# Performance work log

Hardware: AMD Instinct MI355X
Metric: run time of the kernel (lower is better)

Reference implementation:

```python
import jax, jax.numpy as jnp
import numpy as np


def setup_inputs() -> dict:
    key = jax.random.key(0)
    ks = jax.random.split(key, 6)
    B, Tq, Tk = 4, 512, 512
    Q, K, C = 1024, 1024, 256
    query = jax.random.normal(ks[0], (B, Tq, Q), dtype=jnp.float32)
    kmat = jax.random.normal(ks[1], (B, Tk, K), dtype=jnp.float32)
    # Linear weights (torch nn.Linear stores [out, in]; we keep [in, out] for einsum)
    Wq = jax.random.normal(ks[2], (Q, C), dtype=jnp.float32) / np.sqrt(Q)
    Wk = jax.random.normal(ks[3], (K, C), dtype=jnp.float32) / np.sqrt(K)
    w_attn = jax.random.normal(ks[4], (C,), dtype=jnp.float32) / np.sqrt(C)
    b_attn = jax.random.normal(ks[5], (), dtype=jnp.float32) * 0.01
    return {"query": query, "key": kmat, "Wq": Wq, "Wk": Wk,
            "w_attn": w_attn, "b_attn": b_attn}


def reference(query, key, Wq, Wk, w_attn, b_attn):
    # Additive (Bahdanau) attention scores.
    # q2ctx: (B, Tq, C); k2ctx: (B, Tk, C)
    q2ctx = jnp.einsum('bqi,ic->bqc', query, Wq)
    k2ctx = jnp.einsum('bki,ic->bkc', key, Wk)
    # broadcast add -> (B, Tq, Tk, C), tanh, project to scalar and squeeze
    ctx = jnp.tanh(q2ctx[:, :, None, :] + k2ctx[:, None, :, :])
    scores = jnp.einsum('bqkc,c->bqk', ctx, w_attn) + b_attn
    return scores  # (B, Tq, Tk)
```

## Files before the change

### kernel.cpp

```cpp
#include <hip/hip_runtime.h>
#include <hip/hip_bf16.h>

#define M_ROWS 2048
#define KDIM   1024
#define CDIM   256
#define TQ     512
#define TK     512

#define GBM 64
#define GBN 32
#define GBK 32

#define SCALE2LOG2E 2.8853900817779268f

typedef __attribute__((ext_vector_type(8))) short short8;
typedef __attribute__((ext_vector_type(8))) unsigned short ushort8;
typedef __attribute__((ext_vector_type(4))) float floatx4;
typedef __attribute__((ext_vector_type(2))) float f32x2;

__device__ __forceinline__ short2 cvt2(float x, float y) {
    __hip_bfloat162 h = __float22bfloat162_rn(make_float2(x, y));
    short2 r;
    __builtin_memcpy(&r, &h, sizeof(r));
    return r;
}
__device__ __forceinline__ unsigned short f2bf1(float x) {
    return (unsigned short)cvt2(x, x).x;
}
__device__ __forceinline__ float bf2f(unsigned short u) {
    return __builtin_bit_cast(float, (unsigned)u << 16);
}
__device__ __forceinline__ f32x2 splat2(float x) { return (f32x2){x, x}; }

__global__ __launch_bounds__(256) void gemm_mfma_kernel(
    const float* __restrict__ Aq, const float* __restrict__ Ak,
    const float* __restrict__ Wq, const float* __restrict__ Wk,
    const float* __restrict__ w_attn,
    unsigned short* __restrict__ Eq, unsigned short* __restrict__ Ek)
{
    __shared__ short Ws[GBN][GBK + 8];

    const int z = blockIdx.z;
    const float* A = z ? Ak : Aq;
    const float* W = z ? Wk : Wq;
    unsigned short* E = z ? Ek : Eq;

    const int t    = threadIdx.x;
    const int lane = t & 63;
    const int wave = t >> 6;
    const int m0   = blockIdx.x * GBM;
    const int n0   = blockIdx.y * GBN;

    const int wr = t >> 3;
    const int wc = (t & 7) * 4;
    const int li = lane & 15;
    const int qd = lane >> 4;

    const int row = m0 + wave * 16 + li;
    const float* Arow = A + (size_t)row * KDIM + qd * 8;

    floatx4 acc0 = {0.f, 0.f, 0.f, 0.f};
    floatx4 acc1 = {0.f, 0.f, 0.f, 0.f};

    float4 pa0[2], pa1[2], pw[2];
    pa0[0] = *(const float4*)&Arow[0];
    pa1[0] = *(const float4*)&Arow[4];
    pw[0]  = *(const float4*)&W[(size_t)wr * CDIM + n0 + wc];
    pa0[1] = *(const float4*)&Arow[GBK];
    pa1[1] = *(const float4*)&Arow[GBK + 4];
    pw[1]  = *(const float4*)&W[(size_t)(GBK + wr) * CDIM + n0 + wc];

    for (int it = 0; it < KDIM / GBK; ++it) {
        const int s = it & 1;
        __syncthreads();
        short2 u0 = cvt2(pw[s].x, pw[s].y), u1 = cvt2(pw[s].z, pw[s].w);
        Ws[wc + 0][wr] = u0.x;
        Ws[wc + 1][wr] = u0.y;
        Ws[wc + 2][wr] = u1.x;
        Ws[wc + 3][wr] = u1.y;
        short2 p0 = cvt2(pa0[s].x, pa0[s].y), p1 = cvt2(pa0[s].z, pa0[s].w);
        short2 p2 = cvt2(pa1[s].x, pa1[s].y), p3 = cvt2(pa1[s].z, pa1[s].w);
        short8 bv = { p0.x, p0.y, p1.x, p1.y, p2.x, p2.y, p3.x, p3.y };
        __syncthreads();
        if (it + 2 < KDIM / GBK) {
            const int k0 = (it + 2) * GBK;
            pa0[s] = *(const float4*)&Arow[k0];
            pa1[s] = *(const float4*)&Arow[k0 + 4];
            pw[s]  = *(const float4*)&W[(size_t)(k0 + wr) * CDIM + n0 + wc];
        }
        short8 af0 = *(const short8*)&Ws[li][qd * 8];
        short8 af1 = *(const short8*)&Ws[16 + li][qd * 8];
        acc0 = __builtin_amdgcn_mfma_f32_16x16x32_bf16(af0, bv, acc0, 0, 0, 0);
        acc1 = __builtin_amdgcn_mfma_f32_16x16x32_bf16(af1, bv, acc1, 0, 0, 0);
    }

    #pragma unroll
    for (int r = 0; r < 4; ++r) {
        const int c0 = n0 + qd * 4 + r;
        const int c1 = c0 + 16;
        float s0 = z ? 1.0f : (-0.5f / w_attn[c0]);
        float s1 = z ? 1.0f : (-0.5f / w_attn[c1]);
        float v0 = __builtin_amdgcn_exp2f(acc0[r] * SCALE2LOG2E) * s0;
        float v1 = __builtin_amdgcn_exp2f(acc1[r] * SCALE2LOG2E) * s1;
        E[(size_t)c0 * M_ROWS + row] = f2bf1(v0);
        E[(size_t)c1 * M_ROWS + row] = f2bf1(v1);
    }
}

__global__ __launch_bounds__(256) void bahdanau_kernel(
    const unsigned short* __restrict__ Eqs, const unsigned short* __restrict__ Ek,
    const float* __restrict__ w_attn, const float* __restrict__ b_attn,
    float* __restrict__ out)
{
    __shared__ float qs[64][36];
    __shared__ float ks[64][36];
    __shared__ __align__(16) float sl[CDIM];
    __shared__ float partial[4];

    const int t  = threadIdx.x;
    const int b  = blockIdx.z;
    const int q0 = blockIdx.x * 32;
    const int k0 = blockIdx.y * 32;
    const int gq = b * TQ + q0;
    const int gk = b * TK + k0;
    const int tq = (t >> 4) * 2;
    const int tk = (t & 15) * 2;

    const int lr = t >> 2;
    const int lc = (t & 3) * 8;

    {
        float wv = w_attn[t];
        sl[t] = -0.5f / wv;
        float sum = wv;
        #pragma unroll
        for (int o = 32; o >= 1; o >>= 1) sum += __shfl_down(sum, o);
        if ((t & 63) == 0) partial[t >> 6] = sum;
    }

    ushort8 qu = *(const ushort8*)&Eqs[(size_t)lr * M_ROWS + gq + lc];
    ushort8 ku = *(const ushort8*)&Ek [(size_t)lr * M_ROWS + gk + lc];

    f32x2 accA = {0.f, 0.f};
    f32x2 accB = {0.f, 0.f};

    for (int ch = 0; ch < 4; ++ch) {
        __syncthreads();
        *(float4*)&qs[lr][lc]     = make_float4(bf2f(qu[0]), bf2f(qu[1]), bf2f(qu[2]), bf2f(qu[3]));
        *(float4*)&qs[lr][lc + 4] = make_float4(bf2f(qu[4]), bf2f(qu[5]), bf2f(qu[6]), bf2f(qu[7]));
        *(float4*)&ks[lr][lc]     = make_float4(bf2f(ku[0]), bf2f(ku[1]), bf2f(ku[2]), bf2f(ku[3]));
        *(float4*)&ks[lr][lc + 4] = make_float4(bf2f(ku[4]), bf2f(ku[5]), bf2f(ku[6]), bf2f(ku[7]));
        __syncthreads();
        if (ch < 3) {
            const int c1 = (ch + 1) * 64;
            qu = *(const ushort8*)&Eqs[(size_t)(c1 + lr) * M_ROWS + gq + lc];
            ku = *(const ushort8*)&Ek [(size_t)(c1 + lr) * M_ROWS + gk + lc];
        }
        const int cb = ch * 64;
        #pragma unroll
        for (int cc = 0; cc < 64; cc += 4) {
            float4 s4 = *(const float4*)&sl[cb + cc];
            f32x2 q1 = *(const f32x2*)&qs[cc + 0][tq];
            f32x2 q2 = *(const f32x2*)&qs[cc + 1][tq];
            f32x2 q3 = *(const f32x2*)&qs[cc + 2][tq];
            f32x2 q4 = *(const f32x2*)&qs[cc + 3][tq];
            f32x2 k1 = *(const f32x2*)&ks[cc + 0][tk];
            f32x2 k2 = *(const f32x2*)&ks[cc + 1][tk];
            f32x2 k3 = *(const f32x2*)&ks[cc + 2][tk];
            f32x2 k4 = *(const f32x2*)&ks[cc + 3][tk];
            {
                f32x2 f1 = __builtin_elementwise_fma(splat2(q1.x), k1, splat2(s4.x));
                f32x2 f2 = __builtin_elementwise_fma(splat2(q2.x), k2, splat2(s4.y));
                f32x2 f3 = __builtin_elementwise_fma(splat2(q3.x), k3, splat2(s4.z));
                f32x2 f4 = __builtin_elementwise_fma(splat2(q4.x), k4, splat2(s4.w));
                f32x2 p12 = f1 * f2, p34 = f3 * f4;
                f32x2 s12 = f1 + f2, s34 = f3 + f4;
                f32x2 num = __builtin_elementwise_fma(s12, p34, s34 * p12);
                f32x2 den = p12 * p34;
                f32x2 r = {__builtin_amdgcn_rcpf(den.x), __builtin_amdgcn_rcpf(den.y)};
                accA = __builtin_elementwise_fma(num, r, accA);
            }
            {
                f32x2 f1 = __builtin_elementwise_fma(splat2(q1.y), k1, splat2(s4.x));
                f32x2 f2 = __builtin_elementwise_fma(splat2(q2.y), k2, splat2(s4.y));
                f32x2 f3 = __builtin_elementwise_fma(splat2(q3.y), k3, splat2(s4.z));
                f32x2 f4 = __builtin_elementwise_fma(splat2(q4.y), k4, splat2(s4.w));
                f32x2 p12 = f1 * f2, p34 = f3 * f4;
                f32x2 s12 = f1 + f2, s34 = f3 + f4;
                f32x2 num = __builtin_elementwise_fma(s12, p34, s34 * p12);
                f32x2 den = p12 * p34;
                f32x2 r = {__builtin_amdgcn_rcpf(den.x), __builtin_amdgcn_rcpf(den.y)};
                accB = __builtin_elementwise_fma(num, r, accB);
            }
        }
    }

    const float bias2 = *b_attn + partial[0] + partial[1] + partial[2] + partial[3];
    float* o = out + ((size_t)b * TQ + q0 + tq) * TK + k0 + tk;
    *(float2*)&o[0]  = make_float2(accA.x + bias2, accA.y + bias2);
    *(float2*)&o[TK] = make_float2(accB.x + bias2, accB.y + bias2);
}

extern "C" void kernel_launch(void* const* d_in, const int* in_sizes, int n_in,
                              void* d_out, int out_size, void* d_ws, size_t ws_size,
                              hipStream_t stream) {
    const float* query  = (const float*)d_in[0];
    const float* key    = (const float*)d_in[1];
    const float* Wq     = (const float*)d_in[2];
    const float* Wk     = (const float*)d_in[3];
    const float* w_attn = (const float*)d_in[4];
    const float* b_attn = (const float*)d_in[5];
    float* out = (float*)d_out;

    unsigned short* Eqs = (unsigned short*)d_ws;
    unsigned short* Ek  = Eqs + (size_t)CDIM * M_ROWS;

    dim3 gemm_grid(M_ROWS / GBM, CDIM / GBN, 2);
    gemm_mfma_kernel<<<gemm_grid, 256, 0, stream>>>(query, key, Wq, Wk, w_attn, Eqs, Ek);

    dim3 main_grid(TQ / 32, TK / 32, 4);
    bahdanau_kernel<<<main_grid, 256, 0, stream>>>(Eqs, Ek, w_attn, b_attn, out);
}
```

Measured before the change: 109.6 us.

## Deepen GEMM prefetch, double-buffer LDS, and split channels across waves in scorer

Result: slower. 112.1 us (+2.3%).

```diff
diff --git a/kernel.cpp b/kernel.cpp
--- a/kernel.cpp
+++ b/kernel.cpp
@@ -10,6 +10,8 @@
 #define GBM 64
 #define GBN 32
 #define GBK 32
+#define NIT (KDIM / GBK)
+#define DEPTH 4
 
 #define SCALE2LOG2E 2.8853900817779268f
 
@@ -38,7 +40,7 @@
     const float* __restrict__ w_attn,
     unsigned short* __restrict__ Eq, unsigned short* __restrict__ Ek)
 {
-    __shared__ short Ws[GBN][GBK + 8];
+    __shared__ short Ws[2][GBN][GBK + 8];
 
     const int z = blockIdx.z;
     const float* A = z ? Ak : Aq;
@@ -62,36 +64,49 @@
     floatx4 acc0 = {0.f, 0.f, 0.f, 0.f};
     floatx4 acc1 = {0.f, 0.f, 0.f, 0.f};
 
-    float4 pa0[2], pa1[2], pw[2];
-    pa0[0] = *(const float4*)&Arow[0];
-    pa1[0] = *(const float4*)&Arow[4];
-    pw[0]  = *(const float4*)&W[(size_t)wr * CDIM + n0 + wc];
-    pa0[1] = *(const float4*)&Arow[GBK];
-    pa1[1] = *(const float4*)&Arow[GBK + 4];
-    pw[1]  = *(const float4*)&W[(size_t)(GBK + wr) * CDIM + n0 + wc];
-
-    for (int it = 0; it < KDIM / GBK; ++it) {
-        const int s = it & 1;
-        __syncthreads();
-        short2 u0 = cvt2(pw[s].x, pw[s].y), u1 = cvt2(pw[s].z, pw[s].w);
-        Ws[wc + 0][wr] = u0.x;
-        Ws[wc + 1][wr] = u0.y;
-        Ws[wc + 2][wr] = u1.x;
-        Ws[wc + 3][wr] = u1.y;
+    float4 pa0[DEPTH], pa1[DEPTH], pw[DEPTH];
+    #pragma unroll
+    for (int d = 0; d < DEPTH; ++d) {
+        pa0[d] = *(const float4*)&Arow[d * GBK];
+        pa1[d] = *(const float4*)&Arow[d * GBK + 4];
+        pw[d]  = *(const float4*)&W[(size_t)(d * GBK + wr) * CDIM + n0 + wc];
+    }
+
+    {
+        short2 u0 = cvt2(pw[0].x, pw[0].y), u1 = cvt2(pw[0].z, pw[0].w);
+        Ws[0][wc + 0][wr] = u0.x;
+        Ws[0][wc + 1][wr] = u0.y;
+        Ws[0][wc + 2][wr] = u1.x;
+        Ws[0][wc + 3][wr] = u1.y;
+    }
+    __syncthreads();
+
+    #pragma unroll
+    for (int it = 0; it < NIT; ++it) {
+        const int buf = it & 1;
+        const int s   = it & 3;
         short2 p0 = cvt2(pa0[s].x, pa0[s].y), p1 = cvt2(pa0[s].z, pa0[s].w);
         short2 p2 = cvt2(pa1[s].x, pa1[s].y), p3 = cvt2(pa1[s].z, pa1[s].w);
         short8 bv = { p0.x, p0.y, p1.x, p1.y, p2.x, p2.y, p3.x, p3.y };
-        __syncthreads();
-        if (it + 2 < KDIM / GBK) {
-            const int k0 = (it + 2) * GBK;
+        short8 af0 = *(const short8*)&Ws[buf][li][qd * 8];
+        short8 af1 = *(const short8*)&Ws[buf][16 + li][qd * 8];
+        acc0 = __builtin_amdgcn_mfma_f32_16x16x32_bf16(af0, bv, acc0, 0, 0, 0);
+        acc1 = __builtin_amdgcn_mfma_f32_16x16x32_bf16(af1, bv, acc1, 0, 0, 0);
+        if (it + 1 < NIT) {
+            const int ns = (it + 1) & 3;
+            short2 u0 = cvt2(pw[ns].x, pw[ns].y), u1 = cvt2(pw[ns].z, pw[ns].w);
+            Ws[buf ^ 1][wc + 0][wr] = u0.x;
+            Ws[buf ^ 1][wc + 1][wr] = u0.y;
+            Ws[buf ^ 1][wc + 2][wr] = u1.x;
+            Ws[buf ^ 1][wc + 3][wr] = u1.y;
+        }
+        if (it + DEPTH < NIT) {
+            const int k0 = (it + DEPTH) * GBK;
             pa0[s] = *(const float4*)&Arow[k0];
             pa1[s] = *(const float4*)&Arow[k0 + 4];
             pw[s]  = *(const float4*)&W[(size_t)(k0 + wr) * CDIM + n0 + wc];
         }
-        short8 af0 = *(const short8*)&Ws[li][qd * 8];
-        short8 af1 = *(const short8*)&Ws[16 + li][qd * 8];
-        acc0 = __builtin_amdgcn_mfma_f32_16x16x32_bf16(af0, bv, acc0, 0, 0, 0);
-        acc1 = __builtin_amdgcn_mfma_f32_16x16x32_bf16(af1, bv, acc1, 0, 0, 0);
+        __syncthreads();
     }
 
     #pragma unroll
@@ -112,22 +127,23 @@
     const float* __restrict__ w_attn, const float* __restrict__ b_attn,
     float* __restrict__ out)
 {
-    __shared__ float qs[64][36];
-    __shared__ float ks[64][36];
+    __shared__ union SMem {
+        struct { float q[CDIM][36]; float k[CDIM][36]; } s;
+        float red[16][4][64];
+    } sm;
     __shared__ __align__(16) float sl[CDIM];
     __shared__ float partial[4];
 
-    const int t  = threadIdx.x;
-    const int b  = blockIdx.z;
-    const int q0 = blockIdx.x * 32;
-    const int k0 = blockIdx.y * 32;
-    const int gq = b * TQ + q0;
-    const int gk = b * TK + k0;
-    const int tq = (t >> 4) * 2;
-    const int tk = (t & 15) * 2;
-
-    const int lr = t >> 2;
-    const int lc = (t & 3) * 8;
+    const int t    = threadIdx.x;
+    const int b    = blockIdx.z;
+    const int q0g  = blockIdx.x * 32;
+    const int k0g  = blockIdx.y * 32;
+    const int gq   = b * TQ + q0g;
+    const int gk   = b * TK + k0g;
+    const int wave = t >> 6;
+    const int tl   = t & 63;
+    const int q0   = (tl >> 3) * 4;
+    const int k0   = (tl & 7) * 4;
 
     {
         float wv = w_attn[t];
@@ -138,67 +154,88 @@
         if ((t & 63) == 0) partial[t >> 6] = sum;
     }
 
-    ushort8 qu = *(const ushort8*)&Eqs[(size_t)lr * M_ROWS + gq + lc];
-    ushort8 ku = *(const ushort8*)&Ek [(size_t)lr * M_ROWS + gk + lc];
-
-    f32x2 accA = {0.f, 0.f};
-    f32x2 accB = {0.f, 0.f};
-
-    for (int ch = 0; ch < 4; ++ch) {
-        __syncthreads();
-        *(float4*)&qs[lr][lc]     = make_float4(bf2f(qu[0]), bf2f(qu[1]), bf2f(qu[2]), bf2f(qu[3]));
-        *(float4*)&qs[lr][lc + 4] = make_float4(bf2f(qu[4]), bf2f(qu[5]), bf2f(qu[6]), bf2f(qu[7]));
-        *(float4*)&ks[lr][lc]     = make_float4(bf2f(ku[0]), bf2f(ku[1]), bf2f(ku[2]), bf2f(ku[3]));
-        *(float4*)&ks[lr][lc + 4] = make_float4(bf2f(ku[4]), bf2f(ku[5]), bf2f(ku[6]), bf2f(ku[7]));
-        __syncthreads();
-        if (ch < 3) {
-            const int c1 = (ch + 1) * 64;
-            qu = *(const ushort8*)&Eqs[(size_t)(c1 + lr) * M_ROWS + gq + lc];
-            ku = *(const ushort8*)&Ek [(size_t)(c1 + lr) * M_ROWS + gk + lc];
-        }
-        const int cb = ch * 64;
-        #pragma unroll
-        for (int cc = 0; cc < 64; cc += 4) {
-            float4 s4 = *(const float4*)&sl[cb + cc];
-            f32x2 q1 = *(const f32x2*)&qs[cc + 0][tq];
-            f32x2 q2 = *(const f32x2*)&qs[cc + 1][tq];
-            f32x2 q3 = *(const f32x2*)&qs[cc + 2][tq];
-            f32x2 q4 = *(const f32x2*)&qs[cc + 3][tq];
-            f32x2 k1 = *(const f32x2*)&ks[cc + 0][tk];
-            f32x2 k2 = *(const f32x2*)&ks[cc + 1][tk];
-            f32x2 k3 = *(const f32x2*)&ks[cc + 2][tk];
-            f32x2 k4 = *(const f32x2*)&ks[cc + 3][tk];
-            {
-                f32x2 f1 = __builtin_elementwise_fma(splat2(q1.x), k1, splat2(s4.x));
-                f32x2 f2 = __builtin_elementwise_fma(splat2(q2.x), k2, splat2(s4.y));
-                f32x2 f3 = __builtin_elementwise_fma(splat2(q3.x), k3, splat2(s4.z));
-                f32x2 f4 = __builtin_elementwise_fma(splat2(q4.x), k4, splat2(s4.w));
+    const int sr = t >> 2;
+    const int sc = (t & 3) * 8;
+    ushort8 qv[4], kv[4];
+    #pragma unroll
+    for (int p = 0; p < 4; ++p) {
+        qv[p] = *(const ushort8*)&Eqs[(size_t)(p * 64 + sr) * M_ROWS + gq + sc];
+        kv[p] = *(const ushort8*)&Ek [(size_t)(p * 64 + sr) * M_ROWS + gk + sc];
+    }
+    #pragma unroll
+    for (int p = 0; p < 4; ++p) {
+        const int r = p * 64 + sr;
+        *(float4*)&sm.s.q[r][sc]     = make_float4(bf2f(qv[p][0]), bf2f(qv[p][1]), bf2f(qv[p][2]), bf2f(qv[p][3]));
+        *(float4*)&sm.s.q[r][sc + 4] = make_float4(bf2f(qv[p][4]), bf2f(qv[p][5]), bf2f(qv[p][6]), bf2f(qv[p][7]));
+        *(float4*)&sm.s.k[r][sc]     = make_float4(bf2f(kv[p][0]), bf2f(kv[p][1]), bf2f(kv[p][2]), bf2f(kv[p][3]));
+        *(float4*)&sm.s.k[r][sc + 4] = make_float4(bf2f(kv[p][4]), bf2f(kv[p][5]), bf2f(kv[p][6]), bf2f(kv[p][7]));
+    }
+    __syncthreads();
+
+    f32x2 acc[4][2];
+    #pragma unroll
+    for (int qi = 0; qi < 4; ++qi) {
+        acc[qi][0] = (f32x2){0.f, 0.f};
+        acc[qi][1] = (f32x2){0.f, 0.f};
+    }
+    const int cb = wave * 64;
+    #pragma unroll 2
+    for (int cc = 0; cc < 64; cc += 4) {
+        float4 s4 = *(const float4*)&sl[cb + cc];
+        f32x2 qa[4][2], ka[4][2];
+        #pragma unroll
+        for (int j = 0; j < 4; ++j) {
+            qa[j][0] = *(const f32x2*)&sm.s.q[cb + cc + j][q0];
+            qa[j][1] = *(const f32x2*)&sm.s.q[cb + cc + j][q0 + 2];
+            ka[j][0] = *(const f32x2*)&sm.s.k[cb + cc + j][k0];
+            ka[j][1] = *(const f32x2*)&sm.s.k[cb + cc + j][k0 + 2];
+        }
+        #pragma unroll
+        for (int qi = 0; qi < 4; ++qi) {
+            const float qw0 = qa[0][qi >> 1][qi & 1];
+            const float qw1 = qa[1][qi >> 1][qi & 1];
+            const float qw2 = qa[2][qi >> 1][qi & 1];
+            const float qw3 = qa[3][qi >> 1][qi & 1];
+            #pragma unroll
+            for (int kp = 0; kp < 2; ++kp) {
+                f32x2 f1 = __builtin_elementwise_fma(splat2(qw0), ka[0][kp], splat2(s4.x));
+                f32x2 f2 = __builtin_elementwise_fma(splat2(qw1), ka[1][kp], splat2(s4.y));
+                f32x2 f3 = __builtin_elementwise_fma(splat2(qw2), ka[2][kp], splat2(s4.z));
+                f32x2 f4 = __builtin_elementwise_fma(splat2(qw3), ka[3][kp], splat2(s4.w));
                 f32x2 p12 = f1 * f2, p34 = f3 * f4;
                 f32x2 s12 = f1 + f2, s34 = f3 + f4;
                 f32x2 num = __builtin_elementwise_fma(s12, p34, s34 * p12);
                 f32x2 den = p12 * p34;
                 f32x2 r = {__builtin_amdgcn_rcpf(den.x), __builtin_amdgcn_rcpf(den.y)};
-                accA = __builtin_elementwise_fma(num, r, accA);
+                acc[qi][kp] = __builtin_elementwise_fma(num, r, acc[qi][kp]);
             }
-            {
-                f32x2 f1 = __builtin_elementwise_fma(splat2(q1.y), k1, splat2(s4.x));
-                f32x2 f2 = __builtin_elementwise_fma(splat2(q2.y), k2, splat2(s4.y));
-                f32x2 f3 = __builtin_elementwise_fma(splat2(q3.y), k3, splat2(s4.z));
-                f32x2 f4 = __builtin_elementwise_fma(splat2(q4.y), k4, splat2(s4.w));
-                f32x2 p12 = f1 * f2, p34 = f3 * f4;
-                f32x2 s12 = f1 + f2, s34 = f3 + f4;
-                f32x2 num = __builtin_elementwise_fma(s12, p34, s34 * p12);
-                f32x2 den = p12 * p34;
-                f32x2 r = {__builtin_amdgcn_rcpf(den.x), __builtin_amdgcn_rcpf(den.y)};
-                accB = __builtin_elementwise_fma(num, r, accB);
-            }
-        }
-    }
+        }
+    }
+
+    __syncthreads();
+    #pragma unroll
+    for (int qi = 0; qi < 4; ++qi) {
+        #pragma unroll
+        for (int kp = 0; kp < 2; ++kp) {
+            sm.red[qi * 4 + kp * 2 + 0][wave][tl] = acc[qi][kp].x;
+            sm.red[qi * 4 + kp * 2 + 1][wave][tl] = acc[qi][kp].y;
+        }
+    }
+    __syncthreads();
 
     const float bias2 = *b_attn + partial[0] + partial[1] + partial[2] + partial[3];
-    float* o = out + ((size_t)b * TQ + q0 + tq) * TK + k0 + tk;
-    *(float2*)&o[0]  = make_float2(accA.x + bias2, accA.y + bias2);
-    *(float2*)&o[TK] = make_float2(accB.x + bias2, accB.y + bias2);
+    const int L  = t & 63;
+    const int i  = t >> 6;
+    const int qr = (L >> 3) * 4 + i;
+    const int kc = (L & 7) * 4;
+    float4 v;
+    #pragma unroll
+    for (int j = 0; j < 4; ++j) {
+        float s = sm.red[i * 4 + j][0][L] + sm.red[i * 4 + j][1][L]
+                + sm.red[i * 4 + j][2][L] + sm.red[i * 4 + j][3][L];
+        (&v.x)[j] = s + bias2;
+    }
+    *(float4*)&out[((size_t)b * TQ + q0g + qr) * TK + k0g + kc] = v;
 }
 
 extern "C" void kernel_launch(void* const* d_in, const int* in_sizes, int n_in,
```
